# Performance work log

Hardware: AMD Instinct MI355X
Metric: run time of the kernel (lower is better)

## Reference

```python
import jax, jax.numpy as jnp
import numpy as np

B, T, D, H = 2, 2048, 1024, 16
HD = D // H
REG = 16
WIN = 256
ROPE_BASE = 10000.0


def _rope_cos_sin(t, hd):
    theta = 1.0 / (ROPE_BASE ** (jnp.arange(0, hd, 2, dtype=jnp.float32) / hd))  # [hd/2]
    idx_theta = jnp.arange(t, dtype=jnp.float32)[:, None] * theta[None, :]       # [T, hd/2]
    return jnp.cos(idx_theta), jnp.sin(idx_theta)


def _apply_rope(x, cos, sin):
    # x: [B, T, H, HD]
    xs = x.reshape(*x.shape[:-1], HD // 2, 2)
    x0, x1 = xs[..., 0], xs[..., 1]
    c = cos[None, :, None, :]
    s = sin[None, :, None, :]
    out = jnp.stack([x0 * c - x1 * s, x1 * c + x0 * s], axis=-1)
    return out.reshape(x.shape)


def _keep_mask(t):
    # Faithful to _build_attention_register_mask: True = attend (SDPA bool semantics).
    i = jnp.arange(t)[:, None]
    j = jnp.arange(t)[None, :]
    half = WIN // 2
    window_block = (i >= REG) & (j >= jnp.maximum(REG, i - half)) & (j <= i + half)
    blocked = (j < REG) | (i < REG) | window_block
    return ~blocked  # [T, T] bool


def setup_inputs() -> dict:
    key = jax.random.key(0)
    k1, k2, k3 = jax.random.split(key, 3)
    x = jax.random.normal(k1, (B, T, D), dtype=jnp.float32)
    w_attn = jax.random.normal(k2, (3 * D, D), dtype=jnp.float32) * 0.02  # torch Linear weight [out,in]
    w_proj = jax.random.normal(k3, (D, D), dtype=jnp.float32) * 0.02
    return {"x": x, "w_attn": w_attn, "w_proj": w_proj}


def reference(x, w_attn, w_proj):
    b, t, d = x.shape
    qkv = jnp.einsum('btd,ed->bte', x, w_attn)               # [B,T,3D]
    q, k, v = jnp.split(qkv, 3, axis=-1)
    q = q.reshape(b, t, H, HD)
    k = k.reshape(b, t, H, HD)
    v = v.reshape(b, t, H, HD)
    cos, sin = _rope_cos_sin(t, HD)
    q = _apply_rope(q, cos, sin)
    k = _apply_rope(k, cos, sin)
    q = q.transpose(0, 2, 1, 3)  # [B,H,T,HD]
    k = k.transpose(0, 2, 1, 3)
    v = v.transpose(0, 2, 1, 3)
    keep = _keep_mask(t)
    scores = jnp.einsum('bhqd,bhkd->bhqk', q, k) / jnp.sqrt(jnp.float32(HD))
    scores = jnp.where(keep[None, None], scores, -jnp.inf)
    # safe softmax (fully-masked rows -> 0, matching SDPA efficient backends)
    m = jnp.max(scores, axis=-1, keepdims=True)
    m = jnp.where(jnp.isfinite(m), m, 0.0)
    e = jnp.exp(scores - m)
    s = jnp.sum(e, axis=-1, keepdims=True)
    probs = e / jnp.maximum(s, 1e-20)
    y = jnp.einsum('bhqk,bhkd->bhqd', probs, v)
    y = y.transpose(0, 2, 1, 3).reshape(b, t, d)
    return jnp.einsum('btd,ed->bte', y, w_proj)
```

## Files before the change

kernel.cpp:

```cpp
#include <hip/hip_runtime.h>
#include <hip/hip_bf16.h>

#define DEV static __device__ __forceinline__

typedef __attribute__((ext_vector_type(8))) short bf16x8;
typedef __attribute__((ext_vector_type(4))) float f32x4;

#define MFMA16(a, b, c) __builtin_amdgcn_mfma_f32_16x16x32_bf16((a), (b), (c), 0, 0, 0)

#define B_ 2
#define T_ 2048
#define D_ 1024
#define H_ 16
#define HD_ 64
#define LOG2E 1.4426950408889634f

DEV short f2bf(float f) {
  union { float f; unsigned u; } w; w.f = f;
  unsigned u = w.u + 0x7fffu + ((w.u >> 16) & 1u);
  return (short)(u >> 16);
}

DEV void gld16(const void* g, void* l) {
  __builtin_amdgcn_global_load_lds(
      (const __attribute__((address_space(1))) void*)g,
      (__attribute__((address_space(3))) void*)l, 16, 0, 0);
}

#define XN 4194304
#define WAN 3145728
__global__ void cvt_k(const float* __restrict__ x, const float* __restrict__ wa,
                      const float* __restrict__ wp, short* __restrict__ xb,
                      short* __restrict__ wab, short* __restrict__ wpb,
                      float2* __restrict__ tab) {
  size_t gi = ((size_t)blockIdx.x * 256 + threadIdx.x) * 8;
  const float* src; short* dst;
  if (gi < XN) { src = x + gi; dst = xb + gi; }
  else if (gi < XN + WAN) { src = wa + (gi - XN); dst = wab + (gi - XN); }
  else { src = wp + (gi - XN - WAN); dst = wpb + (gi - XN - WAN); }
  float4 a = *(const float4*)src;
  float4 b = *(const float4*)(src + 4);
  bf16x8 o;
  o[0] = f2bf(a.x); o[1] = f2bf(a.y); o[2] = f2bf(a.z); o[3] = f2bf(a.w);
  o[4] = f2bf(b.x); o[5] = f2bf(b.y); o[6] = f2bf(b.z); o[7] = f2bf(b.w);
  *(bf16x8*)dst = o;
  if (blockIdx.x < 256) {
    int i = blockIdx.x * 256 + threadIdx.x;
    int t = i >> 5, d = i & 31;
    float theta = powf(10000.0f, -(float)(2 * d) / 64.0f);
    float ang = (float)t * theta;
    tab[i] = make_float2(cosf(ang), sinf(ang));
  }
}

#define GEMM_CORE(Aptr, Bptr, KDIM)                                              \
  __shared__ short aT[128 * 64];                                                 \
  __shared__ short bT[128 * 64];                                                 \
  const int tid = threadIdx.x;                                                   \
  const int lane = tid & 63, w = tid >> 6;                                       \
  const int l15 = lane & 15, lg = lane >> 4;                                     \
  const int wr = w >> 1, wc = w & 1;                                             \
  const int mBase = blockIdx.y * 128, nBase = blockIdx.x * 128;                  \
  const int lrow = lane >> 3;                                                    \
  const int gch = (lane & 7) ^ lrow;                                             \
  const short* Asrc = (Aptr) + (size_t)(mBase + w * 32 + lrow) * (KDIM) + gch * 8;\
  const short* Bsrc = (Bptr) + (size_t)(nBase + w * 32 + lrow) * (KDIM) + gch * 8;\
  short* aDst = aT + w * 2048;                                                   \
  short* bDst = bT + w * 2048;                                                   \
  f32x4 acc[4][4];                                                               \
  _Pragma("unroll") for (int i = 0; i < 4; ++i)                                  \
  _Pragma("unroll") for (int j = 0; j < 4; ++j)                                  \
      acc[i][j] = (f32x4){0.f, 0.f, 0.f, 0.f};                                   \
  const int nk = (KDIM) / 64;                                                    \
  for (int kt = 0; kt < nk; ++kt) {                                              \
    if (kt) __syncthreads();                                                     \
    _Pragma("unroll") for (int p = 0; p < 4; ++p) {                              \
      gld16(Asrc + kt * 64 + p * 8 * (KDIM), aDst + p * 512);                    \
      gld16(Bsrc + kt * 64 + p * 8 * (KDIM), bDst + p * 512);                    \
    }                                                                            \
    __syncthreads();                \
    bf16x8 af[4][2], bfv[4][2];                                                  \
    _Pragma("unroll") for (int i = 0; i < 4; ++i)                                \
    _Pragma("unroll") for (int s = 0; s < 2; ++s) {                              \
      const int ra = wr * 64 + i * 16 + l15;                                     \
      const int rb = wc * 64 + i * 16 + l15;                                     \
      af[i][s] = *(const bf16x8*)&aT[ra * 64 + (((4 * s + lg) ^ (ra & 7)) * 8)]; \
      bfv[i][s] = *(const bf16x8*)&bT[rb * 64 + (((4 * s + lg) ^ (rb & 7)) * 8)];\
    }                                                                            \
    _Pragma("unroll") for (int mi = 0; mi < 4; ++mi)                             \
    _Pragma("unroll") for (int ni = 0; ni < 4; ++ni)                             \
    _Pragma("unroll") for (int s = 0; s < 2; ++s)                                \
        acc[mi][ni] = MFMA16(af[mi][s], bfv[ni][s], acc[mi][ni]);                \
  }

__global__ void gemm_qkv_k(const short* __restrict__ Xb, const short* __restrict__ Wb,
                           short* __restrict__ Q, short* __restrict__ Ko,
                           short* __restrict__ Vt, const float2* __restrict__ tab) {
  GEMM_CORE(Xb, Wb, 1024)

  const int sec = nBase >> 10;
#pragma unroll
  for (int mi = 0; mi < 4; ++mi) {
    const int m0 = mBase + wr * 64 + mi * 16 + lg * 4;
#pragma unroll
    for (int ni = 0; ni < 4; ++ni) {
      const int n = nBase + wc * 64 + ni * 16 + l15;
      const int hd = n & 63;
      const int h = (n >> 6) & 15;
      if (sec < 2) {
        short* dst = (sec == 0) ? Q : Ko;
        const float qscale = (sec == 0) ? (0.125f * LOG2E) : 1.0f;
#pragma unroll
        for (int r = 0; r < 4; ++r) {
          int m = m0 + r; int b = m >> 11; int t = m & 2047;
          float v = acc[mi][ni][r];
          float pv = __shfl_xor(v, 1);
          float2 cs = tab[t * 32 + (hd >> 1)];
          float o = (lane & 1) ? (v * cs.x + pv * cs.y) : (v * cs.x - pv * cs.y);
          o *= qscale;
          dst[(((size_t)b * H_ + h) * T_ + t) * HD_ + hd] = f2bf(o);
        }
      } else {
        int b = m0 >> 11; int t0 = m0 & 2047;
        short4 s4;
        s4.x = f2bf(acc[mi][ni][0]); s4.y = f2bf(acc[mi][ni][1]);
        s4.z = f2bf(acc[mi][ni][2]); s4.w = f2bf(acc[mi][ni][3]);
        *(short4*)&Vt[(((size_t)b * H_ + h) * HD_ + hd) * T_ + t0] = s4;
      }
    }
  }
}

#define QBLK 128
__global__ __launch_bounds__(512, 4) void attn_k(const short* __restrict__ Qg,
                                                 const short* __restrict__ Kg,
                                                 const short* __restrict__ Vg,
                                                 short* __restrict__ Y) {
  __shared__ short kLds[64 * 72];
  __shared__ short vLds[64 * 72];
  __shared__ short pLds[2 * 64 * 72];
  const int tid = threadIdx.x;
  const int lane = tid & 63, w = tid >> 6;
  const int g = w >> 2, wl = w & 3;
  const int l15 = lane & 15, lg = lane >> 4;
  const int bid = blockIdx.x;
  const int wg = ((bid & 7) << 6) | (bid >> 3);
  const int qt = wg & 15, bh = wg >> 4;
  const int b = bh >> 4, h = bh & 15;
  const int q0 = qt * QBLK;
  const int qg = q0 + g * 64;
  const short* Qh = Qg + (size_t)bh * T_ * HD_;
  const short* Kh = Kg + (size_t)bh * T_ * HD_;
  const short* Vh = Vg + (size_t)bh * HD_ * T_;
  short* pl = pLds + g * 4608;

  bf16x8 qa[2];
  {
    const int qrow = qg + wl * 16 + l15;
    qa[0] = *(const bf16x8*)&Qh[(size_t)qrow * HD_ + lg * 8];
    qa[1] = *(const bf16x8*)&Qh[(size_t)qrow * HD_ + 32 + lg * 8];
  }
  f32x4 o[4];
#pragma unroll
  for (int i = 0; i < 4; ++i) o[i] = (f32x4){0.f, 0.f, 0.f, 0.f};
  float lsum[4] = {0.f, 0.f, 0.f, 0.f};

  const int sRow = tid >> 3, sC = (tid & 7) * 8;
  bf16x8 kreg, vreg;
  auto issueLoad = [&](int kt) {
    const int k0 = kt * 64;
    kreg = *(const bf16x8*)&Kh[(size_t)(k0 + sRow) * HD_ + sC];
    vreg = *(const bf16x8*)&Vh[(size_t)sRow * T_ + k0 + sC];
  };
  auto bothBanned = [&](int kt) { const int k0 = kt * 64; return k0 >= q0 - 1 && k0 <= q0 + 65; };

  const int NT = T_ / 64;
  int kt = 0;
  while (kt < NT && bothBanned(kt)) ++kt;
  issueLoad(kt);

  while (kt < NT) {
    int ktn = kt + 1;
    while (ktn < NT && bothBanned(ktn)) ++ktn;

    __syncthreads();
    *(bf16x8*)&kLds[sRow * 72 + sC] = kreg;
    *(bf16x8*)&vLds[sRow * 72 + sC] = vreg;
    if (ktn < NT) issueLoad(ktn);
    asm volatile("s_waitcnt lgkmcnt(0)" ::: "memory");
    __builtin_amdgcn_s_barrier();

    const int k0 = kt * 64;
    if (!(k0 >= qg - 65 && k0 <= qg + 65)) {
      const bool clean = (qg >= 16) && (k0 >= 16) &&
                         ((k0 + 63 < qg - 128) || (k0 > qg + 63 + 128));

      f32x4 s[4];
#pragma unroll
      for (int i = 0; i < 4; ++i) s[i] = (f32x4){0.f, 0.f, 0.f, 0.f};
#pragma unroll
      for (int nf = 0; nf < 4; ++nf)
#pragma unroll
        for (int ks = 0; ks < 2; ++ks) {
          bf16x8 kb = *(const bf16x8*)&kLds[(nf * 16 + l15) * 72 + ks * 32 + lg * 8];
          s[nf] = MFMA16(qa[ks], kb, s[nf]);
        }

      if (!clean) {
#pragma unroll
        for (int nf = 0; nf < 4; ++nf) {
          const int j = k0 + nf * 16 + l15;
#pragma unroll
          for (int r = 0; r < 4; ++r) {
            const int i = qg + wl * 16 + lg * 4 + r;
            const bool keep = (i >= 16) && (j >= 16) && ((j < i - 128) || (j > i + 128));
            if (!keep) s[nf][r] = -__builtin_inff();
          }
        }
      }

#pragma unroll
      for (int nf = 0; nf < 4; ++nf)
#pragma unroll
        for (int r = 0; r < 4; ++r) {
          float e = __builtin_amdgcn_exp2f(s[nf][r]);
          lsum[r] += e;
          pl[(wl * 16 + lg * 4 + r) * 72 + nf * 16 + l15] = f2bf(e);
        }
#pragma unroll
      for (int nf = 0; nf < 4; ++nf)
#pragma unroll
        for (int ks = 0; ks < 2; ++ks) {
          bf16x8 pa = *(const bf16x8*)&pl[(wl * 16 + l15) * 72 + ks * 32 + lg * 8];
          bf16x8 vb = *(const bf16x8*)&vLds[(nf * 16 + l15) * 72 + ks * 32 + lg * 8];
          o[nf] = MFMA16(pa, vb, o[nf]);
        }
    }
    kt = ktn;
  }

  float rl[4];
#pragma unroll
  for (int r = 0; r < 4; ++r) {
    float v = lsum[r];
    v += __shfl_xor(v, 1);
    v += __shfl_xor(v, 2);
    v += __shfl_xor(v, 4);
    v += __shfl_xor(v, 8);
    rl[r] = 1.0f / fmaxf(v, 1e-20f);
  }
#pragma unroll
  for (int nf = 0; nf < 4; ++nf)
#pragma unroll
    for (int r = 0; r < 4; ++r) {
      const int t = qg + wl * 16 + lg * 4 + r;
      Y[((size_t)(b * T_ + t)) * D_ + h * HD_ + nf * 16 + l15] = f2bf(o[nf][r] * rl[r]);
    }
}

__global__ void gemm_proj_k(const short* __restrict__ Yg, const short* __restrict__ Wb,
                            float* __restrict__ Out) {
  GEMM_CORE(Yg, Wb, 1024)

#pragma unroll
  for (int mi = 0; mi < 4; ++mi)
#pragma unroll
    for (int ni = 0; ni < 4; ++ni)
#pragma unroll
      for (int r = 0; r < 4; ++r)
        Out[(size_t)(mBase + wr * 64 + mi * 16 + lg * 4 + r) * 1024 +
            nBase + wc * 64 + ni * 16 + l15] = acc[mi][ni][r];
}

extern "C" void kernel_launch(void* const* d_in, const int* in_sizes, int n_in,
                              void* d_out, int out_size, void* d_ws, size_t ws_size,
                              hipStream_t stream) {
  const float* x = (const float*)d_in[0];
  const float* w_attn = (const float*)d_in[1];
  const float* w_proj = (const float*)d_in[2];
  float* out = (float*)d_out;
  char* ws = (char*)d_ws;
  char* outc = (char*)d_out;
  short* Q   = (short*)(ws);
  short* K   = (short*)(ws + (size_t)8388608);
  short* Vt  = (short*)(ws + (size_t)16777216);
  short* Y   = (short*)(ws + (size_t)25165824);
  short* Wpb = (short*)(ws + (size_t)33554432);
  short* Xb   = (short*)(outc);
  short* Wab  = (short*)(outc + (size_t)8388608);
  float2* tab = (float2*)(outc + (size_t)14680064);

  cvt_k<<<dim3(4096), dim3(256), 0, stream>>>(x, w_attn, w_proj, Xb, Wab, Wpb, tab);
  gemm_qkv_k<<<dim3(24, 32), dim3(256), 0, stream>>>(Xb, Wab, Q, K, Vt, tab);
  attn_k<<<dim3(B_ * H_ * (T_ / QBLK)), dim3(512), 0, stream>>>(Q, K, Vt, Y);
  gemm_proj_k<<<dim3(8, 32), dim3(256), 0, stream>>>(Y, Wpb, out);
}
```

Baseline: 129.5 us.

## Split attention KV range in two and combine partial outputs in a new kernel

The attention kernel now launches twice as many workgroups, each covering half of the key tiles, and writes unnormalised fp32 partial outputs and row sums to two buffers. A new combine kernel adds the halves, normalises and converts to bf16 for the projection GEMM. The aim is more parallelism and better CU occupancy from the 512 original workgroups. The cost is extra fp32 global traffic, an additional kernel launch, and reuse of the output buffer as scratch.

```diff
diff --git a/kernel.cpp b/kernel.cpp
--- a/kernel.cpp
+++ b/kernel.cpp
@@ -135,7 +135,10 @@
 __global__ __launch_bounds__(512, 4) void attn_k(const short* __restrict__ Qg,
                                                  const short* __restrict__ Kg,
                                                  const short* __restrict__ Vg,
-                                                 short* __restrict__ Y) {
+                                                 float* __restrict__ Oa,
+                                                 float* __restrict__ La,
+                                                 float* __restrict__ Obuf,
+                                                 float* __restrict__ Lb) {
   __shared__ short kLds[64 * 72];
   __shared__ short vLds[64 * 72];
   __shared__ short pLds[2 * 64 * 72];
@@ -144,11 +147,14 @@
   const int g = w >> 2, wl = w & 3;
   const int l15 = lane & 15, lg = lane >> 4;
   const int bid = blockIdx.x;
-  const int wg = ((bid & 7) << 6) | (bid >> 3);
-  const int qt = wg & 15, bh = wg >> 4;
+  const int wg = ((bid & 7) << 7) | (bid >> 3);
+  const int sp = wg & 1;
+  const int qt = (wg >> 1) & 15, bh = wg >> 5;
   const int b = bh >> 4, h = bh & 15;
   const int q0 = qt * QBLK;
   const int qg = q0 + g * 64;
+  float* Op = sp ? Obuf : Oa;
+  float* Lp = sp ? Lb : La;
   const short* Qh = Qg + (size_t)bh * T_ * HD_;
   const short* Kh = Kg + (size_t)bh * T_ * HD_;
   const short* Vh = Vg + (size_t)bh * HD_ * T_;
@@ -174,19 +180,19 @@
   };
   auto bothBanned = [&](int kt) { const int k0 = kt * 64; return k0 >= q0 - 1 && k0 <= q0 + 65; };
 
-  const int NT = T_ / 64;
-  int kt = 0;
-  while (kt < NT && bothBanned(kt)) ++kt;
-  issueLoad(kt);
-
-  while (kt < NT) {
+  const int ktLo = sp * 16, ktHi = ktLo + 16;
+  int kt = ktLo;
+  while (kt < ktHi && bothBanned(kt)) ++kt;
+  if (kt < ktHi) issueLoad(kt);
+
+  while (kt < ktHi) {
     int ktn = kt + 1;
-    while (ktn < NT && bothBanned(ktn)) ++ktn;
+    while (ktn < ktHi && bothBanned(ktn)) ++ktn;
 
     __syncthreads();
     *(bf16x8*)&kLds[sRow * 72 + sC] = kreg;
     *(bf16x8*)&vLds[sRow * 72 + sC] = vreg;
-    if (ktn < NT) issueLoad(ktn);
+    if (ktn < ktHi) issueLoad(ktn);
     asm volatile("s_waitcnt lgkmcnt(0)" ::: "memory");
     __builtin_amdgcn_s_barrier();
 
@@ -239,7 +245,6 @@
     kt = ktn;
   }
 
-  float rl[4];
 #pragma unroll
   for (int r = 0; r < 4; ++r) {
     float v = lsum[r];
@@ -247,15 +252,39 @@
     v += __shfl_xor(v, 2);
     v += __shfl_xor(v, 4);
     v += __shfl_xor(v, 8);
-    rl[r] = 1.0f / fmaxf(v, 1e-20f);
+    if (l15 == 0) {
+      const int t = qg + wl * 16 + lg * 4 + r;
+      Lp[(size_t)bh * T_ + t] = v;
+    }
   }
 #pragma unroll
   for (int nf = 0; nf < 4; ++nf)
 #pragma unroll
     for (int r = 0; r < 4; ++r) {
       const int t = qg + wl * 16 + lg * 4 + r;
-      Y[((size_t)(b * T_ + t)) * D_ + h * HD_ + nf * 16 + l15] = f2bf(o[nf][r] * rl[r]);
+      Op[((size_t)(b * T_ + t)) * D_ + h * HD_ + nf * 16 + l15] = o[nf][r];
     }
+}
+
+__global__ void combine_k(const float* __restrict__ Oa, const float* __restrict__ Ob,
+                          const float* __restrict__ la, const float* __restrict__ lb,
+                          short* __restrict__ Y) {
+  size_t base = ((size_t)blockIdx.x * 256 + threadIdx.x) * 8;
+  const int b = (int)(base >> 21);
+  const int rem = (int)(base & ((1u << 21) - 1));
+  const int t = rem >> 10, d0 = rem & 1023, h = d0 >> 6;
+  const size_t li = (size_t)(b * H_ + h) * T_ + t;
+  const float rl = 1.0f / fmaxf(la[li] + lb[li], 1e-20f);
+  float4 a0 = *(const float4*)&Oa[base];
+  float4 a1 = *(const float4*)&Oa[base + 4];
+  float4 b0 = *(const float4*)&Ob[base];
+  float4 b1 = *(const float4*)&Ob[base + 4];
+  bf16x8 o;
+  o[0] = f2bf((a0.x + b0.x) * rl); o[1] = f2bf((a0.y + b0.y) * rl);
+  o[2] = f2bf((a0.z + b0.z) * rl); o[3] = f2bf((a0.w + b0.w) * rl);
+  o[4] = f2bf((a1.x + b1.x) * rl); o[5] = f2bf((a1.y + b1.y) * rl);
+  o[6] = f2bf((a1.z + b1.z) * rl); o[7] = f2bf((a1.w + b1.w) * rl);
+  *(bf16x8*)&Y[base] = o;
 }
 
 __global__ void gemm_proj_k(const short* __restrict__ Yg, const short* __restrict__ Wb,
@@ -286,12 +315,17 @@
   short* Vt  = (short*)(ws + (size_t)16777216);
   short* Y   = (short*)(ws + (size_t)25165824);
   short* Wpb = (short*)(ws + (size_t)33554432);
+  float* Ob  = (float*)(ws + (size_t)35651584);
+  float* la  = (float*)(ws + (size_t)52428800);
+  float* lb  = (float*)(ws + (size_t)52690944);
   short* Xb   = (short*)(outc);
   short* Wab  = (short*)(outc + (size_t)8388608);
   float2* tab = (float2*)(outc + (size_t)14680064);
+  float* Oa   = (float*)(outc);
 
   cvt_k<<<dim3(4096), dim3(256), 0, stream>>>(x, w_attn, w_proj, Xb, Wab, Wpb, tab);
   gemm_qkv_k<<<dim3(24, 32), dim3(256), 0, stream>>>(Xb, Wab, Q, K, Vt, tab);
-  attn_k<<<dim3(B_ * H_ * (T_ / QBLK)), dim3(512), 0, stream>>>(Q, K, Vt, Y);
+  attn_k<<<dim3(2 * B_ * H_ * (T_ / QBLK)), dim3(512), 0, stream>>>(Q, K, Vt, Oa, la, Ob, lb);
+  combine_k<<<dim3(2048), dim3(256), 0, stream>>>(Oa, Ob, la, lb, Y);
   gemm_proj_k<<<dim3(8, 32), dim3(256), 0, stream>>>(Y, Wpb, out);
 }
```

Result: slower. 137.6 us (+6.3%).
